# Optimization experiments

Hardware: AMD Instinct MI355X
Metric: run time of the kernel (lower is better)

Reference implementation:

```python
import jax, jax.numpy as jnp
import numpy as np

LN_EPS = 1e-5


def setup_inputs() -> dict:
    key = jax.random.key(0)
    ks = jax.random.split(key, 5)
    N, E, D, H = 100000, 1000000, 64, 64
    x = jax.random.normal(ks[0], (N, D), dtype=jnp.float32)
    edge_index = jax.random.randint(ks[1], (2, E), 0, N, dtype=jnp.int64)
    W_l = jax.random.normal(ks[2], (H, D), dtype=jnp.float32) * (1.0 / np.sqrt(D))
    W_r = jax.random.normal(ks[3], (H, D), dtype=jnp.float32) * (1.0 / np.sqrt(D))
    b = jnp.zeros((H,), dtype=jnp.float32)
    gamma = jnp.ones((H,), dtype=jnp.float32)
    beta = jnp.zeros((H,), dtype=jnp.float32)
    return {"x": x, "edge_index": edge_index, "W_l": W_l, "W_r": W_r,
            "b": b, "gamma": gamma, "beta": beta}


def reference(x, edge_index, W_l, W_r, b, gamma, beta):
    N = x.shape[0]
    src, dst = edge_index[0], edge_index[1]
    # mean aggregation of neighbor (source) features at destination nodes
    msg = x[src]                                          # [E, D] gather
    agg = jax.ops.segment_sum(msg, dst, num_segments=N)   # [N, D] scatter-add
    cnt = jax.ops.segment_sum(jnp.ones((src.shape[0],), x.dtype), dst,
                              num_segments=N)             # [N]
    mean = agg / jnp.maximum(cnt, 1.0)[:, None]
    # SAGEConv: lin_l(mean) + lin_r(x), bias on lin_l
    h = mean @ W_l.T + x @ W_r.T + b                      # [N, H]
    # LayerNorm over feature dim
    mu = jnp.mean(h, axis=-1, keepdims=True)
    var = jnp.mean((h - mu) ** 2, axis=-1, keepdims=True)
    hn = (h - mu) / jnp.sqrt(var + LN_EPS) * gamma + beta
    # ELU
    return jnp.where(hn > 0, hn, jnp.expm1(hn))
```

## Files before the change

kernel.cpp:

```cpp
#include <hip/hip_runtime.h>
#include <hip/hip_bf16.h>

#define LN_EPS 1e-5f
#define BSH   7
#define BNODE 128
#define EPB   8192
#define CAP   4096

typedef __attribute__((ext_vector_type(8))) short bf16x8;
typedef __attribute__((ext_vector_type(4))) float floatx4;

#define F2BF(f) ((unsigned short)((__float_as_uint(f) + 0x7FFF + \
                ((__float_as_uint(f) >> 16) & 1)) >> 16))

__global__ __launch_bounds__(256) void cvt_kernel(
    const float* __restrict__ x, unsigned short* __restrict__ xb, int n64,
    int* __restrict__ bcount, int NB)
{
    if (blockIdx.x == 0) {
        for (int i = threadIdx.x; i < NB; i += 256) bcount[i] = 0;
    }
    int i = (blockIdx.x * 256 + threadIdx.x) * 8;
    if (i >= n64) return;
    float4 a = *(const float4*)&x[i];
    float4 b = *(const float4*)&x[i + 4];
    uint4 o;
    o.x = (unsigned)F2BF(a.x) | ((unsigned)F2BF(a.y) << 16);
    o.y = (unsigned)F2BF(a.z) | ((unsigned)F2BF(a.w) << 16);
    o.z = (unsigned)F2BF(b.x) | ((unsigned)F2BF(b.y) << 16);
    o.w = (unsigned)F2BF(b.z) | ((unsigned)F2BF(b.w) << 16);
    *(uint4*)&xb[i] = o;
}

__global__ __launch_bounds__(256) void bucket_hist_kernel(
    const int* __restrict__ ei, int* __restrict__ bcount, int E, int NB)
{
    __shared__ int lhist[1024];
    int t = threadIdx.x;
    int base = blockIdx.x * EPB;
    for (int b = t; b < NB; b += 256) lhist[b] = 0;
    __syncthreads();
    #pragma unroll 4
    for (int i = 0; i < EPB / 256; ++i) {
        int e = base + i * 256 + t;
        if (e < E) atomicAdd(&lhist[ei[E + e] >> BSH], 1);
    }
    __syncthreads();
    for (int b = t; b < NB; b += 256) {
        int c = lhist[b];
        if (c) atomicAdd(&bcount[b], c);
    }
}

__global__ __launch_bounds__(256) void bucket_scan_kernel(
    const int* __restrict__ bcount, int* __restrict__ bbase,
    int* __restrict__ gcursor, int NB, int E)
{
    __shared__ int wsum[4];
    int t = threadIdx.x;
    int v[4]; int tsum = 0;
    #pragma unroll
    for (int i = 0; i < 4; ++i) {
        int idx = t * 4 + i;
        v[i] = (idx < NB) ? bcount[idx] : 0;
        tsum += v[i];
    }
    int lane = t & 63, w = t >> 6;
    int sc = tsum;
    #pragma unroll
    for (int off = 1; off < 64; off <<= 1) {
        int y = __shfl_up(sc, off);
        if (lane >= off) sc += y;
    }
    if (lane == 63) wsum[w] = sc;
    __syncthreads();
    int woff = 0;
    for (int j = 0; j < w; ++j) woff += wsum[j];
    int run = woff + sc - tsum;
    #pragma unroll
    for (int i = 0; i < 4; ++i) {
        int idx = t * 4 + i;
        if (idx < NB) { bbase[idx] = run; gcursor[idx] = run; }
        run += v[i];
    }
    if (t == 255) bbase[NB] = E;
}

__global__ __launch_bounds__(256) void bucket_scatter_kernel(
    const int* __restrict__ ei,
    int* __restrict__ gcursor,
    int* __restrict__ ebuf,
    int E, int NB)
{
    __shared__ int lhist[1024];
    __shared__ int lbase[1024];
    __shared__ int lcur[1024];

    int t = threadIdx.x;
    int base = blockIdx.x * EPB;

    for (int b = t; b < NB; b += 256) lhist[b] = 0;
    __syncthreads();

    #pragma unroll 4
    for (int i = 0; i < EPB / 256; ++i) {
        int e = base + i * 256 + t;
        if (e < E) atomicAdd(&lhist[ei[E + e] >> BSH], 1);
    }
    __syncthreads();

    for (int b = t; b < NB; b += 256) {
        int c = lhist[b];
        lbase[b] = c ? atomicAdd(&gcursor[b], c) : 0;
        lcur[b]  = 0;
    }
    __syncthreads();

    #pragma unroll 4
    for (int i = 0; i < EPB / 256; ++i) {
        int e = base + i * 256 + t;
        if (e < E) {
            int src = ei[e];
            int dst = ei[E + e];
            int b   = dst >> BSH;
            int pos = lbase[b] + atomicAdd(&lcur[b], 1);
            ebuf[pos] = src | ((dst & (BNODE - 1)) << 17);
        }
    }
}

__global__ __launch_bounds__(256) void csrsort_kernel(
    const int* __restrict__ bbase,
    const int* __restrict__ ebuf,
    int* __restrict__ esrc,
    int* __restrict__ rowstart,
    int N)
{
    __shared__ int lcnt[BNODE];
    __shared__ int lpre[BNODE + 1];
    __shared__ int lcur[BNODE];
    __shared__ int sorted[CAP];

    int t    = threadIdx.x;
    int b    = blockIdx.x;
    int nb0  = b << BSH;
    int nloc = min(BNODE, N - nb0);
    int s0   = bbase[b];
    int s1   = bbase[b + 1];
    int cnt  = s1 - s0;

    if (t < BNODE) { lcnt[t] = 0; lcur[t] = 0; }
    __syncthreads();

    for (int i = s0 + t; i < s1; i += 256)
        atomicAdd(&lcnt[(unsigned)ebuf[i] >> 17], 1);
    __syncthreads();

    if (t < 64) {
        int v0 = lcnt[2 * t], v1 = lcnt[2 * t + 1];
        int p = v0 + v1, sc = p;
        #pragma unroll
        for (int off = 1; off < 64; off <<= 1) {
            int y = __shfl_up(sc, off);
            if (t >= off) sc += y;
        }
        int excl = sc - p;
        lpre[2 * t]     = excl;
        lpre[2 * t + 1] = excl + v0;
        if (t == 63) lpre[BNODE] = excl + p;
    }
    __syncthreads();

    if (t <= nloc) rowstart[nb0 + t] = s0 + lpre[t];

    if (cnt <= CAP) {
        for (int i = s0 + t; i < s1; i += 256) {
            int p = ebuf[i];
            int n = (unsigned)p >> 17;
            int slot = lpre[n] + atomicAdd(&lcur[n], 1);
            sorted[slot] = p & 0x1FFFF;
        }
        __syncthreads();
        for (int i = t; i < cnt; i += 256) esrc[s0 + i] = sorted[i];
    } else {
        for (int i = s0 + t; i < s1; i += 256) {
            int p = ebuf[i];
            int n = (unsigned)p >> 17;
            int slot = s0 + lpre[n] + atomicAdd(&lcur[n], 1);
            esrc[slot] = p & 0x1FFFF;
        }
    }
}

__global__ __launch_bounds__(256) void gather_kernel(
    const unsigned short* __restrict__ xb,
    const int*   __restrict__ rowstart,
    const int*   __restrict__ esrc,
    float* __restrict__ mean,
    int N)
{
    int tid  = threadIdx.x;
    int lane = tid & 63;
    int g    = lane >> 4;
    int sub  = lane & 15;
    int node = blockIdx.x * 4 + (tid >> 6);
    if (node >= N) return;
    int s0 = rowstart[node], s1 = rowstart[node + 1];

    float a0 = 0.f, a1 = 0.f, a2 = 0.f, a3 = 0.f;
    float b0 = 0.f, b1 = 0.f, b2 = 0.f, b3 = 0.f;
    int e = s0 + g;
    for (; e + 4 < s1; e += 8) {
        int sA = esrc[e];
        int sB = esrc[e + 4];
        uint2 va = *(const uint2*)&xb[(size_t)sA * 64 + sub * 4];
        uint2 vb = *(const uint2*)&xb[(size_t)sB * 64 + sub * 4];
        a0 += __uint_as_float(va.x << 16);
        a1 += __uint_as_float(va.x & 0xFFFF0000u);
        a2 += __uint_as_float(va.y << 16);
        a3 += __uint_as_float(va.y & 0xFFFF0000u);
        b0 += __uint_as_float(vb.x << 16);
        b1 += __uint_as_float(vb.x & 0xFFFF0000u);
        b2 += __uint_as_float(vb.y << 16);
        b3 += __uint_as_float(vb.y & 0xFFFF0000u);
    }
    if (e < s1) {
        uint2 va = *(const uint2*)&xb[(size_t)esrc[e] * 64 + sub * 4];
        a0 += __uint_as_float(va.x << 16);
        a1 += __uint_as_float(va.x & 0xFFFF0000u);
        a2 += __uint_as_float(va.y << 16);
        a3 += __uint_as_float(va.y & 0xFFFF0000u);
    }
    a0 += b0; a1 += b1; a2 += b2; a3 += b3;

    a0 += __shfl_xor(a0, 32); a1 += __shfl_xor(a1, 32);
    a2 += __shfl_xor(a2, 32); a3 += __shfl_xor(a3, 32);
    a0 += __shfl_xor(a0, 16); a1 += __shfl_xor(a1, 16);
    a2 += __shfl_xor(a2, 16); a3 += __shfl_xor(a3, 16);

    if (g == 0) {
        float inv = 1.0f / fmaxf((float)(s1 - s0), 1.0f);
        float4 r = make_float4(a0 * inv, a1 * inv, a2 * inv, a3 * inv);
        *(float4*)&mean[(size_t)node * 64 + sub * 4] = r;
    }
}

__global__ __launch_bounds__(256) void mfma_mlp_kernel(
    const unsigned short* __restrict__ xb,
    const float* mean,
    const float* __restrict__ Wl,
    const float* __restrict__ Wr,
    const float* __restrict__ bias,
    const float* __restrict__ gamma,
    const float* __restrict__ beta,
    float* out,
    int N)
{
    __shared__ short smA[64][136];
    __shared__ short smB[64][136];

    int tid  = threadIdx.x;
    int lane = tid & 63;
    int w    = tid >> 6;
    int lo   = lane & 15;
    int hi   = lane >> 4;
    int nbase = blockIdx.x * 64;

    #pragma unroll
    for (int it = 0; it < 4; ++it) {
        int slot = tid + it * 256;
        int row  = slot >> 4;
        int c4   = (slot & 15) * 4;
        int g    = nbase + row;
        size_t roff = (size_t)(g < N ? g : 0) * 64 + c4;
        float4 mv = *(const float4*)&mean[roff];
        float4 wl = *(const float4*)&Wl[slot * 4];
        float4 wr = *(const float4*)&Wr[slot * 4];
        uint2 mp, lp, rp;
        mp.x = (unsigned)F2BF(mv.x) | ((unsigned)F2BF(mv.y) << 16);
        mp.y = (unsigned)F2BF(mv.z) | ((unsigned)F2BF(mv.w) << 16);
        lp.x = (unsigned)F2BF(wl.x) | ((unsigned)F2BF(wl.y) << 16);
        lp.y = (unsigned)F2BF(wl.z) | ((unsigned)F2BF(wl.w) << 16);
        rp.x = (unsigned)F2BF(wr.x) | ((unsigned)F2BF(wr.y) << 16);
        rp.y = (unsigned)F2BF(wr.z) | ((unsigned)F2BF(wr.w) << 16);
        *(uint2*)&smA[row][c4]      = mp;
        *(uint2*)&smB[row][c4]      = lp;
        *(uint2*)&smB[row][64 + c4] = rp;
    }
    #pragma unroll
    for (int it = 0; it < 2; ++it) {
        int s   = tid + it * 256;
        int row = s >> 3;
        int o8  = (s & 7) * 8;
        int g   = nbase + row;
        uint4 v = *(const uint4*)&xb[(size_t)(g < N ? g : 0) * 64 + o8];
        *(uint4*)&smA[row][64 + o8] = v;
    }
    __syncthreads();

    bf16x8 a0 = *(const bf16x8*)&smA[w * 16 + lo][ 0 + hi * 8];
    bf16x8 a1 = *(const bf16x8*)&smA[w * 16 + lo][32 + hi * 8];
    bf16x8 a2 = *(const bf16x8*)&smA[w * 16 + lo][64 + hi * 8];
    bf16x8 a3 = *(const bf16x8*)&smA[w * 16 + lo][96 + hi * 8];

    floatx4 c[4];
    #pragma unroll
    for (int ct = 0; ct < 4; ++ct) {
        float b = bias[ct * 16 + lo];
        c[ct] = (floatx4){b, b, b, b};
    }

    #pragma unroll
    for (int ct = 0; ct < 4; ++ct) {
        int j = ct * 16 + lo;
        bf16x8 b0 = *(const bf16x8*)&smB[j][ 0 + hi * 8];
        bf16x8 b1 = *(const bf16x8*)&smB[j][32 + hi * 8];
        bf16x8 b2 = *(const bf16x8*)&smB[j][64 + hi * 8];
        bf16x8 b3 = *(const bf16x8*)&smB[j][96 + hi * 8];
        c[ct] = __builtin_amdgcn_mfma_f32_16x16x32_bf16(a0, b0, c[ct], 0, 0, 0);
        c[ct] = __builtin_amdgcn_mfma_f32_16x16x32_bf16(a1, b1, c[ct], 0, 0, 0);
        c[ct] = __builtin_amdgcn_mfma_f32_16x16x32_bf16(a2, b2, c[ct], 0, 0, 0);
        c[ct] = __builtin_amdgcn_mfma_f32_16x16x32_bf16(a3, b3, c[ct], 0, 0, 0);
    }

    float s[4], q[4];
    #pragma unroll
    for (int p = 0; p < 4; ++p) {
        s[p] = c[0][p] + c[1][p] + c[2][p] + c[3][p];
        q[p] = c[0][p]*c[0][p] + c[1][p]*c[1][p]
             + c[2][p]*c[2][p] + c[3][p]*c[3][p];
        #pragma unroll
        for (int off = 1; off < 16; off <<= 1) {
            s[p] += __shfl_xor(s[p], off);
            q[p] += __shfl_xor(q[p], off);
        }
    }

    #pragma unroll
    for (int p = 0; p < 4; ++p) {
        int node = nbase + w * 16 + hi * 4 + p;
        if (node >= N) continue;
        float mu  = s[p] * (1.0f / 64.0f);
        float var = q[p] * (1.0f / 64.0f) - mu * mu;
        float rr  = rsqrtf(var + LN_EPS);
        #pragma unroll
        for (int ct = 0; ct < 4; ++ct) {
            int col = ct * 16 + lo;
            float hn = (c[ct][p] - mu) * rr * gamma[col] + beta[col];
            hn = hn > 0.f ? hn : __expf(hn) - 1.0f;
            out[(size_t)node * 64 + col] = hn;
        }
    }
}

extern "C" void kernel_launch(void* const* d_in, const int* in_sizes, int n_in,
                              void* d_out, int out_size, void* d_ws, size_t ws_size,
                              hipStream_t stream) {
    const float* x     = (const float*)d_in[0];
    const int*   ei    = (const int*)  d_in[1];
    const float* Wl    = (const float*)d_in[2];
    const float* Wr    = (const float*)d_in[3];
    const float* bias  = (const float*)d_in[4];
    const float* gamma = (const float*)d_in[5];
    const float* beta  = (const float*)d_in[6];

    int N  = in_sizes[0] / 64;
    int E  = in_sizes[1] / 2;
    int NB = (N + BNODE - 1) >> BSH;

    unsigned short* xb = (unsigned short*)d_ws;
    int* bcount   = (int*)(xb + (size_t)N * 64);
    int* bbase    = bcount + NB;
    int* gcursor  = bbase + (NB + 1);
    int* rowstart = gcursor + NB;
    int* ebuf     = rowstart + (N + 1);
    int* esrc     = ebuf + E;
    float* mean   = (float*)d_out;

    cvt_kernel<<<(N * 64 + 2047) / 2048, 256, 0, stream>>>(x, xb, N * 64,
                                                           bcount, NB);

    int ebl = (E + EPB - 1) / EPB;
    bucket_hist_kernel<<<ebl, 256, 0, stream>>>(ei, bcount, E, NB);

    bucket_scan_kernel<<<1, 256, 0, stream>>>(bcount, bbase, gcursor, NB, E);

    bucket_scatter_kernel<<<ebl, 256, 0, stream>>>(ei, gcursor, ebuf, E, NB);

    csrsort_kernel<<<NB, 256, 0, stream>>>(bbase, ebuf, esrc, rowstart, N);

    gather_kernel<<<(N + 3) / 4, 256, 0, stream>>>(xb, rowstart, esrc, mean, N);

    mfma_mlp_kernel<<<(N + 63) / 64, 256, 0, stream>>>(xb, mean, Wl, Wr, bias,
                                                       gamma, beta,
                                                       (float*)d_out, N);
}
```

Measured before the change: 103.9 us.

## Fuse conversion with edge histogram and store neighbor mean in bf16

Merges the x-to-bf16 conversion kernel and the bucket histogram kernel into one launch, with the histogram work done by the first ebl blocks, and replaces the in-kernel bcount zeroing with a memset. The gather kernel now writes the mean as bf16 into workspace instead of fp32 into the output buffer, which halves that write and the later read in the MLP kernel. This removes one launch and some memory traffic, at the cost of an extra memset call and heavier leading blocks in the fused kernel.

```diff
diff --git a/kernel.cpp b/kernel.cpp
--- a/kernel.cpp
+++ b/kernel.cpp
@@ -13,42 +13,39 @@
 #define F2BF(f) ((unsigned short)((__float_as_uint(f) + 0x7FFF + \
                 ((__float_as_uint(f) >> 16) & 1)) >> 16))
 
-__global__ __launch_bounds__(256) void cvt_kernel(
+__global__ __launch_bounds__(256) void cvt_hist_kernel(
     const float* __restrict__ x, unsigned short* __restrict__ xb, int n64,
-    int* __restrict__ bcount, int NB)
-{
-    if (blockIdx.x == 0) {
-        for (int i = threadIdx.x; i < NB; i += 256) bcount[i] = 0;
-    }
-    int i = (blockIdx.x * 256 + threadIdx.x) * 8;
-    if (i >= n64) return;
-    float4 a = *(const float4*)&x[i];
-    float4 b = *(const float4*)&x[i + 4];
-    uint4 o;
-    o.x = (unsigned)F2BF(a.x) | ((unsigned)F2BF(a.y) << 16);
-    o.y = (unsigned)F2BF(a.z) | ((unsigned)F2BF(a.w) << 16);
-    o.z = (unsigned)F2BF(b.x) | ((unsigned)F2BF(b.y) << 16);
-    o.w = (unsigned)F2BF(b.z) | ((unsigned)F2BF(b.w) << 16);
-    *(uint4*)&xb[i] = o;
-}
-
-__global__ __launch_bounds__(256) void bucket_hist_kernel(
-    const int* __restrict__ ei, int* __restrict__ bcount, int E, int NB)
+    const int* __restrict__ ei, int* __restrict__ bcount, int E, int NB, int ebl)
 {
     __shared__ int lhist[1024];
     int t = threadIdx.x;
-    int base = blockIdx.x * EPB;
-    for (int b = t; b < NB; b += 256) lhist[b] = 0;
-    __syncthreads();
-    #pragma unroll 4
-    for (int i = 0; i < EPB / 256; ++i) {
-        int e = base + i * 256 + t;
-        if (e < E) atomicAdd(&lhist[ei[E + e] >> BSH], 1);
-    }
-    __syncthreads();
-    for (int b = t; b < NB; b += 256) {
-        int c = lhist[b];
-        if (c) atomicAdd(&bcount[b], c);
+
+    if ((int)blockIdx.x < ebl) {
+        for (int b = t; b < NB; b += 256) lhist[b] = 0;
+        __syncthreads();
+        int base = blockIdx.x * EPB;
+        #pragma unroll 4
+        for (int i = 0; i < EPB / 256; ++i) {
+            int e = base + i * 256 + t;
+            if (e < E) atomicAdd(&lhist[ei[E + e] >> BSH], 1);
+        }
+        __syncthreads();
+        for (int b = t; b < NB; b += 256) {
+            int c = lhist[b];
+            if (c) atomicAdd(&bcount[b], c);
+        }
+    }
+
+    int i = (blockIdx.x * 256 + t) * 8;
+    if (i < n64) {
+        float4 a = *(const float4*)&x[i];
+        float4 b = *(const float4*)&x[i + 4];
+        uint4 o;
+        o.x = (unsigned)F2BF(a.x) | ((unsigned)F2BF(a.y) << 16);
+        o.y = (unsigned)F2BF(a.z) | ((unsigned)F2BF(a.w) << 16);
+        o.z = (unsigned)F2BF(b.x) | ((unsigned)F2BF(b.y) << 16);
+        o.w = (unsigned)F2BF(b.z) | ((unsigned)F2BF(b.w) << 16);
+        *(uint4*)&xb[i] = o;
     }
 }
 
@@ -196,7 +193,7 @@
     const unsigned short* __restrict__ xb,
     const int*   __restrict__ rowstart,
     const int*   __restrict__ esrc,
-    float* __restrict__ mean,
+    unsigned short* __restrict__ meanb,
     int N)
 {
     int tid  = threadIdx.x;
@@ -240,20 +237,23 @@
 
     if (g == 0) {
         float inv = 1.0f / fmaxf((float)(s1 - s0), 1.0f);
-        float4 r = make_float4(a0 * inv, a1 * inv, a2 * inv, a3 * inv);
-        *(float4*)&mean[(size_t)node * 64 + sub * 4] = r;
+        float m0 = a0 * inv, m1 = a1 * inv, m2 = a2 * inv, m3 = a3 * inv;
+        uint2 o;
+        o.x = (unsigned)F2BF(m0) | ((unsigned)F2BF(m1) << 16);
+        o.y = (unsigned)F2BF(m2) | ((unsigned)F2BF(m3) << 16);
+        *(uint2*)&meanb[(size_t)node * 64 + sub * 4] = o;
     }
 }
 
 __global__ __launch_bounds__(256) void mfma_mlp_kernel(
     const unsigned short* __restrict__ xb,
-    const float* mean,
+    const unsigned short* __restrict__ meanb,
     const float* __restrict__ Wl,
     const float* __restrict__ Wr,
     const float* __restrict__ bias,
     const float* __restrict__ gamma,
     const float* __restrict__ beta,
-    float* out,
+    float* __restrict__ out,
     int N)
 {
     __shared__ short smA[64][136];
@@ -271,19 +271,13 @@
         int slot = tid + it * 256;
         int row  = slot >> 4;
         int c4   = (slot & 15) * 4;
-        int g    = nbase + row;
-        size_t roff = (size_t)(g < N ? g : 0) * 64 + c4;
-        float4 mv = *(const float4*)&mean[roff];
         float4 wl = *(const float4*)&Wl[slot * 4];
         float4 wr = *(const float4*)&Wr[slot * 4];
-        uint2 mp, lp, rp;
-        mp.x = (unsigned)F2BF(mv.x) | ((unsigned)F2BF(mv.y) << 16);
-        mp.y = (unsigned)F2BF(mv.z) | ((unsigned)F2BF(mv.w) << 16);
+        uint2 lp, rp;
         lp.x = (unsigned)F2BF(wl.x) | ((unsigned)F2BF(wl.y) << 16);
         lp.y = (unsigned)F2BF(wl.z) | ((unsigned)F2BF(wl.w) << 16);
         rp.x = (unsigned)F2BF(wr.x) | ((unsigned)F2BF(wr.y) << 16);
         rp.y = (unsigned)F2BF(wr.z) | ((unsigned)F2BF(wr.w) << 16);
-        *(uint2*)&smA[row][c4]      = mp;
         *(uint2*)&smB[row][c4]      = lp;
         *(uint2*)&smB[row][64 + c4] = rp;
     }
@@ -292,9 +286,11 @@
         int s   = tid + it * 256;
         int row = s >> 3;
         int o8  = (s & 7) * 8;
-        int g   = nbase + row;
-        uint4 v = *(const uint4*)&xb[(size_t)(g < N ? g : 0) * 64 + o8];
-        *(uint4*)&smA[row][64 + o8] = v;
+        size_t roff = (size_t)(nbase + row < N ? nbase + row : 0) * 64 + o8;
+        uint4 vm = *(const uint4*)&meanb[roff];
+        uint4 vx = *(const uint4*)&xb[roff];
+        *(uint4*)&smA[row][o8]      = vm;
+        *(uint4*)&smA[row][64 + o8] = vx;
     }
     __syncthreads();
 
@@ -368,20 +364,21 @@
     int E  = in_sizes[1] / 2;
     int NB = (N + BNODE - 1) >> BSH;
 
-    unsigned short* xb = (unsigned short*)d_ws;
-    int* bcount   = (int*)(xb + (size_t)N * 64);
+    unsigned short* xb    = (unsigned short*)d_ws;
+    unsigned short* meanb = xb + (size_t)N * 64;
+    int* bcount   = (int*)(meanb + (size_t)N * 64);
     int* bbase    = bcount + NB;
     int* gcursor  = bbase + (NB + 1);
     int* rowstart = gcursor + NB;
     int* ebuf     = rowstart + (N + 1);
     int* esrc     = ebuf + E;
-    float* mean   = (float*)d_out;
-
-    cvt_kernel<<<(N * 64 + 2047) / 2048, 256, 0, stream>>>(x, xb, N * 64,
-                                                           bcount, NB);
+
+    hipMemsetAsync(bcount, 0, (size_t)NB * sizeof(int), stream);
 
     int ebl = (E + EPB - 1) / EPB;
-    bucket_hist_kernel<<<ebl, 256, 0, stream>>>(ei, bcount, E, NB);
+    int cvtbl = (N * 64 + 2047) / 2048;
+    cvt_hist_kernel<<<cvtbl, 256, 0, stream>>>(x, xb, N * 64, ei, bcount,
+                                               E, NB, ebl);
 
     bucket_scan_kernel<<<1, 256, 0, stream>>>(bcount, bbase, gcursor, NB, E);
 
@@ -389,9 +386,9 @@
 
     csrsort_kernel<<<NB, 256, 0, stream>>>(bbase, ebuf, esrc, rowstart, N);
 
-    gather_kernel<<<(N + 3) / 4, 256, 0, stream>>>(xb, rowstart, esrc, mean, N);
-
-    mfma_mlp_kernel<<<(N + 63) / 64, 256, 0, stream>>>(xb, mean, Wl, Wr, bias,
+    gather_kernel<<<(N + 3) / 4, 256, 0, stream>>>(xb, rowstart, esrc, meanb, N);
+
+    mfma_mlp_kernel<<<(N + 63) / 64, 256, 0, stream>>>(xb, meanb, Wl, Wr, bias,
                                                        gamma, beta,
                                                        (float*)d_out, N);
 }
```

Result: no change. 105.4 us (+1.4%).
